# Kernel optimization log

Measured on AMD Instinct MI355X. Metric: run time of the kernel, lower is better.

## Reference

```python
import jax, jax.numpy as jnp
import numpy as np

KY, KX = 3, 3  # kernel_size from init_kwargs


def setup_inputs() -> dict:
    key = jax.random.key(0)
    x = jax.random.normal(key, (8, 64, 256, 256), dtype=jnp.float32)
    return {"x": x}


def reference(x):
    # NMS: mask = x > max over 3x3 replicate-padded neighborhood EXCLUDING center.
    # Note: the torch conv kernel zeroes the center row, so the center output
    # channel is all zeros and the max implicitly includes 0 — we replicate that
    # by initializing the running max to zeros.
    ky, kx = KY, KX
    py, px = (ky - 1) // 2, (kx - 1) // 2
    H, W = x.shape[-2], x.shape[-1]
    xp = jnp.pad(x, ((0, 0), (0, 0), (py, py), (px, px)), mode='edge')  # replicate pad
    numel = ky * kx
    center = numel // 2
    max_non_center = jnp.zeros_like(x)  # zeroed-center channel participates in max
    for i in range(numel):  # fixed small kernel window, unrolled (8 shifts)
        if i == center:
            continue
        dy, dx = divmod(i, kx)
        max_non_center = jnp.maximum(max_non_center, xp[..., dy:dy + H, dx:dx + W])
    mask = x > max_non_center
    return x * mask.astype(x.dtype)
```

## Files before the change

kernel.cpp:

```cpp
#include <hip/hip_runtime.h>


#define NMS_H 256
#define NMS_W 256
#define PLANE (NMS_H * NMS_W)
#define ROWS 16

typedef float f4_t __attribute__((ext_vector_type(4)));

struct HV {
    float4 h;
    float4 lr;
};

__device__ __forceinline__ HV rowmax(const float4 v, const int tx) {
    float l = __shfl_up(v.w, 1, 64);
    float r = __shfl_down(v.x, 1, 64);
    if (tx == 0)  l = v.x;
    if (tx == 63) r = v.w;
    HV o;
    o.h.x = fmaxf(l,   fmaxf(v.x, v.y));
    o.h.y = fmaxf(v.x, fmaxf(v.y, v.z));
    o.h.z = fmaxf(v.y, fmaxf(v.z, v.w));
    o.h.w = fmaxf(v.z, fmaxf(v.w, r));
    o.lr.x = fmaxf(l,   v.y);
    o.lr.y = fmaxf(v.x, v.z);
    o.lr.z = fmaxf(v.y, v.w);
    o.lr.w = fmaxf(v.z, r);
    return o;
}

__global__ __launch_bounds__(256) void nms2d_kernel(const float* __restrict__ x,
                                                    float* __restrict__ out) {
    const int tx   = threadIdx.x;
    const int col4 = tx * 4;
    const int gid  = blockIdx.x * blockDim.y + threadIdx.y;
    const int plane_idx = gid >> 4;
    const int r0        = (gid & 15) * ROWS;

    const float* pl = x   + (size_t)plane_idx * PLANE;
    float*       op = out + (size_t)plane_idx * PLANE;

    float4 v[ROWS + 2];
    #pragma unroll
    for (int i = 0; i < ROWS + 2; ++i) {
        const int r = min(max(r0 + i - 1, 0), NMS_H - 1);
        v[i] = *reinterpret_cast<const float4*>(pl + r * NMS_W + col4);
    }
    __builtin_amdgcn_sched_barrier(0);

    HV a = rowmax(v[0], tx);
    HV b = rowmax(v[1], tx);

    #pragma unroll
    for (int i = 0; i < ROWS; ++i) {
        HV c = rowmax(v[i + 2], tx);
        const float4 ctr = v[i + 1];
        f4_t o;
        float m;
        m = fmaxf(0.0f, fmaxf(fmaxf(a.h.x, c.h.x), b.lr.x)); o.x = (ctr.x > m) ? ctr.x : 0.0f;
        m = fmaxf(0.0f, fmaxf(fmaxf(a.h.y, c.h.y), b.lr.y)); o.y = (ctr.y > m) ? ctr.y : 0.0f;
        m = fmaxf(0.0f, fmaxf(fmaxf(a.h.z, c.h.z), b.lr.z)); o.z = (ctr.z > m) ? ctr.z : 0.0f;
        m = fmaxf(0.0f, fmaxf(fmaxf(a.h.w, c.h.w), b.lr.w)); o.w = (ctr.w > m) ? ctr.w : 0.0f;

        *reinterpret_cast<f4_t*>(op + (r0 + i) * NMS_W + col4) = o;

        a = b; b = c;
    }
}

extern "C" void kernel_launch(void* const* d_in, const int* in_sizes, int n_in,
                              void* d_out, int out_size, void* d_ws, size_t ws_size,
                              hipStream_t stream) {
    const float* x = (const float*)d_in[0];
    float* out = (float*)d_out;

    dim3 block(64, 4);
    dim3 grid(2048);
    nms2d_kernel<<<grid, block, 0, stream>>>(x, out);
}
```

Before: 234.1 us.

## Double-buffer row strips into LDS via direct global-to-LDS loads

Each wave now processes 64 rows as eight 8-row strips. The next strip is prefetched into a double-buffered LDS region with global_load_lds while the current one is computed, and stores switch to nontemporal. Blocks shrink to 2 waves and the grid halves, so each wave covers more rows. The aim is to overlap memory latency with compute and cut halo re-reads, at the cost of LDS traffic, a manual vmcnt wait that must match the issued load count, and fewer waves in flight.

Result: no change. 237.3 us (+1.3%).

```diff
diff --git a/kernel.cpp b/kernel.cpp
--- a/kernel.cpp
+++ b/kernel.cpp
@@ -4,9 +4,14 @@
 #define NMS_H 256
 #define NMS_W 256
 #define PLANE (NMS_H * NMS_W)
-#define ROWS 16
+#define SROWS 8
+#define LROWS 10
+#define NSTRIPS 8
+#define BUF_WORDS (LROWS * NMS_W)
 
 typedef float f4_t __attribute__((ext_vector_type(4)));
+typedef __attribute__((address_space(3))) float lds_f;
+typedef const __attribute__((address_space(1))) float glob_f;
 
 struct HV {
     float4 h;
@@ -30,42 +35,68 @@
     return o;
 }
 
-__global__ __launch_bounds__(256) void nms2d_kernel(const float* __restrict__ x,
+__device__ __forceinline__ void dma_strip(const float* pl, int r0,
+                                          lds_f* buf, int col4) {
+    #pragma unroll
+    for (int j = 0; j < LROWS; ++j) {
+        const int r = min(max(r0 + j - 1, 0), NMS_H - 1);
+        glob_f* g = (glob_f*)(pl + r * NMS_W + col4);
+        __builtin_amdgcn_global_load_lds(g, buf + j * NMS_W, 16, 0, 0);
+    }
+}
+
+__global__ __launch_bounds__(128) void nms2d_kernel(const float* __restrict__ x,
                                                     float* __restrict__ out) {
+    __shared__ float lds[2][2][BUF_WORDS];
+
     const int tx   = threadIdx.x;
+    const int ty   = threadIdx.y;
     const int col4 = tx * 4;
-    const int gid  = blockIdx.x * blockDim.y + threadIdx.y;
-    const int plane_idx = gid >> 4;
-    const int r0        = (gid & 15) * ROWS;
+    const int w    = blockIdx.x * 2 + ty;
+    const int plane_idx = w >> 2;
+    const int row_base  = (w & 3) * (NSTRIPS * SROWS);
 
     const float* pl = x   + (size_t)plane_idx * PLANE;
     float*       op = out + (size_t)plane_idx * PLANE;
 
-    float4 v[ROWS + 2];
-    #pragma unroll
-    for (int i = 0; i < ROWS + 2; ++i) {
-        const int r = min(max(r0 + i - 1, 0), NMS_H - 1);
-        v[i] = *reinterpret_cast<const float4*>(pl + r * NMS_W + col4);
-    }
-    __builtin_amdgcn_sched_barrier(0);
+    lds_f* buf0 = (lds_f*)&lds[ty][0][0];
+    lds_f* buf1 = (lds_f*)&lds[ty][1][0];
 
-    HV a = rowmax(v[0], tx);
-    HV b = rowmax(v[1], tx);
+    dma_strip(pl, row_base, buf0, col4);
 
     #pragma unroll
-    for (int i = 0; i < ROWS; ++i) {
-        HV c = rowmax(v[i + 2], tx);
-        const float4 ctr = v[i + 1];
-        f4_t o;
-        float m;
-        m = fmaxf(0.0f, fmaxf(fmaxf(a.h.x, c.h.x), b.lr.x)); o.x = (ctr.x > m) ? ctr.x : 0.0f;
-        m = fmaxf(0.0f, fmaxf(fmaxf(a.h.y, c.h.y), b.lr.y)); o.y = (ctr.y > m) ? ctr.y : 0.0f;
-        m = fmaxf(0.0f, fmaxf(fmaxf(a.h.z, c.h.z), b.lr.z)); o.z = (ctr.z > m) ? ctr.z : 0.0f;
-        m = fmaxf(0.0f, fmaxf(fmaxf(a.h.w, c.h.w), b.lr.w)); o.w = (ctr.w > m) ? ctr.w : 0.0f;
+    for (int s = 0; s < NSTRIPS; ++s) {
+        lds_f* cur = (s & 1) ? buf1 : buf0;
+        lds_f* nxt = (s & 1) ? buf0 : buf1;
 
-        *reinterpret_cast<f4_t*>(op + (r0 + i) * NMS_W + col4) = o;
+        if (s + 1 < NSTRIPS) {
+            dma_strip(pl, row_base + (s + 1) * SROWS, nxt, col4);
+            asm volatile("s_waitcnt vmcnt(10)" ::: "memory");
+        } else {
+            asm volatile("s_waitcnt vmcnt(0)" ::: "memory");
+        }
 
-        a = b; b = c;
+        float4 v[LROWS];
+        #pragma unroll
+        for (int j = 0; j < LROWS; ++j)
+            v[j] = *reinterpret_cast<const float4*>((const float*)(cur + j * NMS_W + col4));
+
+        HV a = rowmax(v[0], tx);
+        HV b = rowmax(v[1], tx);
+        #pragma unroll
+        for (int i = 0; i < SROWS; ++i) {
+            HV c = rowmax(v[i + 2], tx);
+            const float4 ctr = v[i + 1];
+            f4_t o;
+            float m;
+            m = fmaxf(0.0f, fmaxf(fmaxf(a.h.x, c.h.x), b.lr.x)); o.x = (ctr.x > m) ? ctr.x : 0.0f;
+            m = fmaxf(0.0f, fmaxf(fmaxf(a.h.y, c.h.y), b.lr.y)); o.y = (ctr.y > m) ? ctr.y : 0.0f;
+            m = fmaxf(0.0f, fmaxf(fmaxf(a.h.z, c.h.z), b.lr.z)); o.z = (ctr.z > m) ? ctr.z : 0.0f;
+            m = fmaxf(0.0f, fmaxf(fmaxf(a.h.w, c.h.w), b.lr.w)); o.w = (ctr.w > m) ? ctr.w : 0.0f;
+            __builtin_nontemporal_store(o,
+                reinterpret_cast<f4_t*>(op + (row_base + s * SROWS + i) * NMS_W + col4));
+            a = b; b = c;
+        }
     }
 }
 
@@ -75,7 +106,7 @@
     const float* x = (const float*)d_in[0];
     float* out = (float*)d_out;
 
-    dim3 block(64, 4);
-    dim3 grid(2048);
+    dim3 block(64, 2);
+    dim3 grid(1024);
     nms2d_kernel<<<grid, block, 0, stream>>>(x, out);
 }
```

## Process one output row per wavefront with XCD-aware block remapping

Applied to the files above, without the earlier changes.

Replaces the 16-row-per-wave register sliding window with one output row per wave, which loads its three neighbouring rows directly. The grid grows to 32768 blocks, and block indices are remapped so that consecutive logical blocks are spread across the 8 XCDs while neighbouring row groups still share L2. This raises parallelism and occupancy and cuts register pressure. The cost is roughly 3x redundant global/L2 reads of input rows.

After: 226.0 us. 1.04x faster.

```diff
diff --git a/kernel.cpp b/kernel.cpp
--- a/kernel.cpp
+++ b/kernel.cpp
@@ -4,7 +4,6 @@
 #define NMS_H 256
 #define NMS_W 256
 #define PLANE (NMS_H * NMS_W)
-#define ROWS 16
 
 typedef float f4_t __attribute__((ext_vector_type(4)));
 
@@ -32,41 +31,35 @@
 
 __global__ __launch_bounds__(256) void nms2d_kernel(const float* __restrict__ x,
                                                     float* __restrict__ out) {
-    const int tx   = threadIdx.x;
-    const int col4 = tx * 4;
-    const int gid  = blockIdx.x * blockDim.y + threadIdx.y;
-    const int plane_idx = gid >> 4;
-    const int r0        = (gid & 15) * ROWS;
+    const int blk     = blockIdx.x;
+    const int logical = (blk >> 3) + (blk & 7) * (32768 / 8);
 
-    const float* pl = x   + (size_t)plane_idx * PLANE;
-    float*       op = out + (size_t)plane_idx * PLANE;
+    const int plane_idx = logical >> 6;
+    const int rg        = logical & 63;
+    const int tx        = threadIdx.x & 63;
+    const int r         = rg * 4 + (threadIdx.x >> 6);
+    const int col4      = tx * 4;
 
-    float4 v[ROWS + 2];
-    #pragma unroll
-    for (int i = 0; i < ROWS + 2; ++i) {
-        const int r = min(max(r0 + i - 1, 0), NMS_H - 1);
-        v[i] = *reinterpret_cast<const float4*>(pl + r * NMS_W + col4);
-    }
-    __builtin_amdgcn_sched_barrier(0);
+    const float* pl = x + (size_t)plane_idx * PLANE;
 
-    HV a = rowmax(v[0], tx);
-    HV b = rowmax(v[1], tx);
+    const int rm = max(r - 1, 0);
+    const int rp = min(r + 1, NMS_H - 1);
+    const float4 va = *reinterpret_cast<const float4*>(pl + rm * NMS_W + col4);
+    const float4 vc = *reinterpret_cast<const float4*>(pl + r  * NMS_W + col4);
+    const float4 vb = *reinterpret_cast<const float4*>(pl + rp * NMS_W + col4);
 
-    #pragma unroll
-    for (int i = 0; i < ROWS; ++i) {
-        HV c = rowmax(v[i + 2], tx);
-        const float4 ctr = v[i + 1];
-        f4_t o;
-        float m;
-        m = fmaxf(0.0f, fmaxf(fmaxf(a.h.x, c.h.x), b.lr.x)); o.x = (ctr.x > m) ? ctr.x : 0.0f;
-        m = fmaxf(0.0f, fmaxf(fmaxf(a.h.y, c.h.y), b.lr.y)); o.y = (ctr.y > m) ? ctr.y : 0.0f;
-        m = fmaxf(0.0f, fmaxf(fmaxf(a.h.z, c.h.z), b.lr.z)); o.z = (ctr.z > m) ? ctr.z : 0.0f;
-        m = fmaxf(0.0f, fmaxf(fmaxf(a.h.w, c.h.w), b.lr.w)); o.w = (ctr.w > m) ? ctr.w : 0.0f;
+    const HV ma = rowmax(va, tx);
+    const HV mc = rowmax(vc, tx);
+    const HV mb = rowmax(vb, tx);
 
-        *reinterpret_cast<f4_t*>(op + (r0 + i) * NMS_W + col4) = o;
+    f4_t o;
+    float m;
+    m = fmaxf(0.0f, fmaxf(fmaxf(ma.h.x, mb.h.x), mc.lr.x)); o.x = (vc.x > m) ? vc.x : 0.0f;
+    m = fmaxf(0.0f, fmaxf(fmaxf(ma.h.y, mb.h.y), mc.lr.y)); o.y = (vc.y > m) ? vc.y : 0.0f;
+    m = fmaxf(0.0f, fmaxf(fmaxf(ma.h.z, mb.h.z), mc.lr.z)); o.z = (vc.z > m) ? vc.z : 0.0f;
+    m = fmaxf(0.0f, fmaxf(fmaxf(ma.h.w, mb.h.w), mc.lr.w)); o.w = (vc.w > m) ? vc.w : 0.0f;
 
-        a = b; b = c;
-    }
+    *reinterpret_cast<f4_t*>(out + (size_t)plane_idx * PLANE + r * NMS_W + col4) = o;
 }
 
 extern "C" void kernel_launch(void* const* d_in, const int* in_sizes, int n_in,
@@ -75,7 +68,7 @@
     const float* x = (const float*)d_in[0];
     float* out = (float*)d_out;
 
-    dim3 block(64, 4);
-    dim3 grid(2048);
+    dim3 block(256);
+    dim3 grid(32768);
     nms2d_kernel<<<grid, block, 0, stream>>>(x, out);
 }
```
